# Performance work log

Measured on AMD Instinct MI355X. Metric: run time of the kernel, lower is better.

The kernel has to match this reference:

```python
import jax, jax.numpy as jnp
import numpy as np

N_NODES = 50000
N_EDGES = 800000
D = 128
N_LAYERS = 3


def setup_inputs() -> dict:
    key = jax.random.key(0)
    k = jax.random.split(key, 6)
    x = jax.random.normal(k[0], (N_NODES, D), dtype=jnp.float32)
    edge_index = jax.random.randint(k[1], (2, N_EDGES), 0, N_NODES, dtype=jnp.int64)
    scale = 1.0 / np.sqrt(D)
    # SAGEConv params per layer: lin_l (aggregated neighbors, with bias), lin_r (root)
    W_l = jax.random.uniform(k[2], (N_LAYERS, D, D), jnp.float32, -scale, scale)
    b_l = jax.random.uniform(k[3], (N_LAYERS, D), jnp.float32, -scale, scale)
    W_r = jax.random.uniform(k[4], (N_LAYERS, D, D), jnp.float32, -scale, scale)
    return {"x": x, "edge_index": edge_index, "W_l": W_l, "b_l": b_l, "W_r": W_r}


def _sage_layer(x, src, dst, inv_deg, Wl, bl, Wr):
    # gather source-node features, mean-aggregate into destination nodes
    msg = x[src]                                            # [E, D]
    agg = jax.ops.segment_sum(msg, dst, num_segments=N_NODES) * inv_deg  # [N, D]
    # out = lin_l(agg) + lin_r(x)
    return agg @ Wl.T + bl + x @ Wr.T


def reference(x, edge_index, W_l, b_l, W_r):
    src = edge_index[0]
    dst = edge_index[1]
    deg = jax.ops.segment_sum(jnp.ones((src.shape[0],), x.dtype), dst,
                              num_segments=N_NODES)
    inv_deg = (1.0 / jnp.maximum(deg, 1.0))[:, None]        # [N, 1]
    h = x
    for i in range(N_LAYERS):
        h = _sage_layer(h, src, dst, inv_deg, W_l[i], b_l[i], W_r[i])
        if i < N_LAYERS - 1:
            h = jax.nn.relu(h)  # dropout=0.0 -> identity
    return h
```

## Files before the change

### kernel.cpp

```cpp
#include <hip/hip_runtime.h>

#define N_NODES 50000
#define N_EDGES 800000
#define D 128
#define N_LAYERS 3
#define NBUCK ((N_NODES + 255) / 256)

typedef __attribute__((ext_vector_type(8))) short bfrag;
typedef __attribute__((ext_vector_type(4))) float f32x4;
typedef __attribute__((ext_vector_type(8))) unsigned short u16x8;

__device__ __forceinline__ unsigned short f2bf_rn(float f) {
    union { float f; unsigned u; } a; a.f = f;
    unsigned r = a.u + 0x7fffu + ((a.u >> 16) & 1u);
    return (unsigned short)(r >> 16);
}
__device__ __forceinline__ float bf2f(unsigned short h) {
    union { unsigned u; float f; } a; a.u = ((unsigned)h) << 16;
    return a.f;
}
__device__ __forceinline__ unsigned short f2h(float f) {
    union { unsigned short s[1]; _Float16 h; } a; a.h = (_Float16)f; return a.s[0];
}
__device__ __forceinline__ float h2f(unsigned short u) {
    union { unsigned short s[1]; _Float16 h; } a; a.s[0] = u; return (float)a.h;
}

#define GLOAD16(g, l) __builtin_amdgcn_global_load_lds( \
    (const __attribute__((address_space(1))) void*)(g), \
    (__attribute__((address_space(3))) void*)(l), 16, 0, 0)

__global__ void detect_dtype_kernel(const unsigned int* __restrict__ edge, int* __restrict__ flag,
                                    int* __restrict__ gcoarse) {
    __shared__ int any_nz;
    if (threadIdx.x == 0) any_nz = 0;
    __syncthreads();
    int nz = 0;
    for (int i = threadIdx.x; i < 2048; i += blockDim.x) {
        if (edge[2 * i + 1] != 0u) nz = 1;
    }
    if (nz) atomicOr(&any_nz, 1);
    for (int i = threadIdx.x; i < NBUCK; i += blockDim.x) gcoarse[i] = 0;
    __syncthreads();
    if (threadIdx.x == 0) *flag = any_nz ? 0 : 1;
}

__global__ __launch_bounds__(256) void hist_coarse_kernel(const int* __restrict__ edge,
                                                          const int* __restrict__ flag,
                                                          int* __restrict__ gcoarse) {
    __shared__ int h[NBUCK];
    const int t = threadIdx.x;
    for (int i = t; i < NBUCK; i += 256) h[i] = 0;
    __syncthreads();
    const int flagv = *flag;
    const int base = blockIdx.x * 1024;
#pragma unroll
    for (int j = 0; j < 4; ++j) {
        int i = base + j * 256 + t;
        if (i < N_EDGES) {
            int d = flagv ? edge[2 * ((size_t)N_EDGES + i)] : edge[N_EDGES + i];
            atomicAdd(&h[d >> 8], 1);
        }
    }
    __syncthreads();
    for (int i = t; i < NBUCK; i += 256)
        if (h[i]) atomicAdd(&gcoarse[i], h[i]);
}

__global__ __launch_bounds__(256) void scan196_kernel(const int* __restrict__ gcoarse,
                                                      int* __restrict__ bucket_base,
                                                      int* __restrict__ cursor1) {
    __shared__ int s[256];
    int t = threadIdx.x;
    int v = (t < NBUCK) ? gcoarse[t] : 0;
    s[t] = v;
    __syncthreads();
    for (int off = 1; off < 256; off <<= 1) {
        int u = (t >= off) ? s[t - off] : 0;
        __syncthreads();
        s[t] += u;
        __syncthreads();
    }
    if (t < NBUCK) {
        int excl = s[t] - v;
        bucket_base[t] = excl;
        cursor1[t] = excl;
    }
    if (t == 255) bucket_base[NBUCK] = s[255];
}

__global__ __launch_bounds__(256) void pass1_kernel(const int* __restrict__ edge,
                                                    const int* __restrict__ flag,
                                                    int* __restrict__ cursor1,
                                                    int* __restrict__ packed) {
    __shared__ int hist[NBUCK];
    __shared__ int base[NBUCK];
    const int t = threadIdx.x;
    const int flagv = *flag;
    const int blockBeg = blockIdx.x * 4096;
    for (int i = t; i < NBUCK; i += 256) hist[i] = 0;
    __syncthreads();
    int es[16], ed[16];
#pragma unroll
    for (int j = 0; j < 16; ++j) {
        int e = blockBeg + j * 256 + t;
        if (e < N_EDGES) {
            if (flagv) { es[j] = edge[2 * (size_t)e]; ed[j] = edge[2 * ((size_t)N_EDGES + e)]; }
            else       { es[j] = edge[e];             ed[j] = edge[N_EDGES + e]; }
        } else ed[j] = -1;
    }
#pragma unroll
    for (int j = 0; j < 16; ++j)
        if (ed[j] >= 0) atomicAdd(&hist[ed[j] >> 8], 1);
    __syncthreads();
    for (int i = t; i < NBUCK; i += 256) {
        base[i] = atomicAdd(&cursor1[i], hist[i]);
        hist[i] = 0;
    }
    __syncthreads();
#pragma unroll
    for (int j = 0; j < 16; ++j) {
        if (ed[j] >= 0) {
            int b = ed[j] >> 8;
            int pos = base[b] + atomicAdd(&hist[b], 1);
            packed[pos] = ((ed[j] & 255) << 18) | es[j];
        }
    }
}

__global__ __launch_bounds__(256) void build_csr_kernel(const int* __restrict__ bucket_base,
                                                        const int* __restrict__ packed,
                                                        int* __restrict__ offsets,
                                                        float* __restrict__ inv_deg,
                                                        int* __restrict__ csr) {
    __shared__ int cnt[256];
    __shared__ int s[256];
    const int t = threadIdx.x;
    const int b = blockIdx.x;
    const int base = bucket_base[b];
    const int endb = bucket_base[b + 1];
    cnt[t] = 0;
    __syncthreads();
    for (int e = base + t; e < endb; e += 256)
        atomicAdd(&cnt[((unsigned)packed[e]) >> 18], 1);
    __syncthreads();
    int v = cnt[t];
    s[t] = v;
    __syncthreads();
    for (int off = 1; off < 256; off <<= 1) {
        int u = (t >= off) ? s[t - off] : 0;
        __syncthreads();
        s[t] += u;
        __syncthreads();
    }
    int excl = base + s[t] - v;
    int node = b * 256 + t;
    if (node < N_NODES) {
        offsets[node] = excl;
        inv_deg[node] = 1.0f / (float)max(v, 1);
    }
    if (b == NBUCK - 1 && t == 0) offsets[N_NODES] = N_EDGES;
    cnt[t] = excl;
    __syncthreads();
    for (int e = base + t; e < endb; e += 256) {
        int p = packed[e];
        int pos = atomicAdd(&cnt[((unsigned)p) >> 18], 1);
        csr[pos] = p & 0x3FFFF;
    }
}

__global__ void prep_w_kernel(const float* __restrict__ Wl, const float* __restrict__ Wr,
                              unsigned short* __restrict__ WH, unsigned short* __restrict__ WL) {
    int idx = blockIdx.x * blockDim.x + threadIdx.x;
    if (idx >= N_LAYERS * 128 * 256) return;
    int k = idx & 255;
    int j = (idx >> 8) & 127;
    int l = idx >> 15;
    float v = (k < 128) ? Wl[((size_t)l * 128 + j) * 128 + k]
                        : Wr[((size_t)l * 128 + j) * 128 + (k - 128)];
    unsigned short hi = f2bf_rn(v);
    WH[idx] = hi;
    WL[idx] = f2bf_rn(v - bf2f(hi));
}

__global__ void split_x_kernel(const float* __restrict__ x,
                               unsigned short* __restrict__ H16, unsigned short* __restrict__ R16) {
    int t = blockIdx.x * 256 + threadIdx.x;
    if (t >= N_NODES * 32) return;
    float4 v = reinterpret_cast<const float4*>(x)[t];
    ushort4 h, r;
    h.x = f2h(v.x); r.x = f2h(v.x - h2f(h.x));
    h.y = f2h(v.y); r.y = f2h(v.y - h2f(h.y));
    h.z = f2h(v.z); r.z = f2h(v.z - h2f(h.z));
    h.w = f2h(v.w); r.w = f2h(v.w - h2f(h.w));
    reinterpret_cast<ushort4*>(H16)[t] = h;
    reinterpret_cast<ushort4*>(R16)[t] = r;
}

__global__ __launch_bounds__(256) void aggregate_kernel(const unsigned short* __restrict__ hF16,
                                                        const int* __restrict__ offsets,
                                                        const int* __restrict__ csr_src,
                                                        const float* __restrict__ inv_deg,
                                                        unsigned short* __restrict__ aggH,
                                                        unsigned short* __restrict__ aggL) {
    int node = blockIdx.x * 4 + (threadIdx.x >> 6);
    int lane = threadIdx.x & 63;
    int q = lane >> 4;
    int c = lane & 15;
    if (node >= N_NODES) return;
    int beg = offsets[node];
    int end = offsets[node + 1];
    float a0[8], a1[8];
#pragma unroll
    for (int j = 0; j < 8; ++j) { a0[j] = 0.f; a1[j] = 0.f; }
    int e = beg + q;
    for (; e + 4 < end; e += 8) {
        int s0 = csr_src[e];
        int s1 = csr_src[e + 4];
        u16x8 v0 = *reinterpret_cast<const u16x8*>(hF16 + (size_t)s0 * 128 + c * 8);
        u16x8 v1 = *reinterpret_cast<const u16x8*>(hF16 + (size_t)s1 * 128 + c * 8);
#pragma unroll
        for (int j = 0; j < 8; ++j) {
            a0[j] += h2f(v0[j]);
            a1[j] += h2f(v1[j]);
        }
    }
    if (e < end) {
        int s0 = csr_src[e];
        u16x8 v0 = *reinterpret_cast<const u16x8*>(hF16 + (size_t)s0 * 128 + c * 8);
#pragma unroll
        for (int j = 0; j < 8; ++j) a0[j] += h2f(v0[j]);
    }
#pragma unroll
    for (int j = 0; j < 8; ++j) a0[j] += a1[j];
#pragma unroll
    for (int j = 0; j < 8; ++j) a0[j] += __shfl_xor(a0[j], 16, 64);
#pragma unroll
    for (int j = 0; j < 8; ++j) a0[j] += __shfl_xor(a0[j], 32, 64);
    if (q == 0) {
        float w = inv_deg[node];
        u16x8 hi, lo;
#pragma unroll
        for (int j = 0; j < 8; ++j) {
            float v = a0[j] * w;
            hi[j] = f2bf_rn(v);
            lo[j] = f2bf_rn(v - bf2f(hi[j]));
        }
        *reinterpret_cast<u16x8*>(aggH + (size_t)node * 128 + c * 8) = hi;
        *reinterpret_cast<u16x8*>(aggL + (size_t)node * 128 + c * 8) = lo;
    }
}

template <int RELU, int LAST>
__global__ __launch_bounds__(256) void mfma_gemm_kernel(
    const unsigned short* __restrict__ aggH, const unsigned short* __restrict__ aggL,
    const unsigned short* h16, const unsigned short* r16,
    const unsigned short* __restrict__ WH, const unsigned short* __restrict__ WL,
    const float* __restrict__ bias,
    float* __restrict__ OutF, unsigned short* H16o, unsigned short* R16o)
{
    __shared__ __align__(16) unsigned short Bh[4][128][8];
    __shared__ __align__(16) unsigned short Bl[4][128][8];
    const int tid = threadIdx.x;
    const int lane = tid & 63;
    const int wv = tid >> 6;
    const int m16 = lane & 15;
    const int kg = lane >> 4;
    const int blockRow = blockIdx.x * 64;
    const int rowg = blockRow + wv * 16 + m16;
    const int rowc = min(rowg, N_NODES - 1);

    f32x4 acc[8];
#pragma unroll
    for (int t = 0; t < 8; ++t) acc[t] = (f32x4){0.f, 0.f, 0.f, 0.f};

    for (int ks = 0; ks < 8; ++ks) {
        const int kc = ks * 32;
        const int kcol = kc & 127;
        bfrag a_h, a_l;
        if (kc < 128) {
            a_h = *reinterpret_cast<const bfrag*>(aggH + (size_t)rowc * 128 + kcol + kg * 8);
            a_l = *reinterpret_cast<const bfrag*>(aggL + (size_t)rowc * 128 + kcol + kg * 8);
        } else {
            u16x8 hv = *reinterpret_cast<const u16x8*>(h16 + (size_t)rowc * 128 + kcol + kg * 8);
            u16x8 rv = *reinterpret_cast<const u16x8*>(r16 + (size_t)rowc * 128 + kcol + kg * 8);
#pragma unroll
            for (int j = 0; j < 8; ++j) {
                float v = h2f(hv[j]) + h2f(rv[j]);
                union { float f; unsigned u; } a; a.f = v;
                unsigned hu = a.u & 0xFFFF0000u;
                a_h[j] = (short)(hu >> 16);
                union { unsigned u; float f; } b; b.u = hu;
                a_l[j] = (short)f2bf_rn(v - b.f);
            }
        }
        {
            const unsigned short* g0 = WH + (size_t)lane * 256 + kc + wv * 8;
            const unsigned short* g1 = WH + (size_t)(64 + lane) * 256 + kc + wv * 8;
            GLOAD16(g0, (char*)&Bh[0][0][0] + wv * 2048);
            GLOAD16(g1, (char*)&Bh[0][0][0] + wv * 2048 + 1024);
            const unsigned short* g2 = WL + (size_t)lane * 256 + kc + wv * 8;
            const unsigned short* g3 = WL + (size_t)(64 + lane) * 256 + kc + wv * 8;
            GLOAD16(g2, (char*)&Bl[0][0][0] + wv * 2048);
            GLOAD16(g3, (char*)&Bl[0][0][0] + wv * 2048 + 1024);
        }
        __syncthreads();
#pragma unroll
        for (int t = 0; t < 8; ++t) {
            bfrag bh = *reinterpret_cast<const bfrag*>(&Bh[kg][t * 16 + m16][0]);
            bfrag bl = *reinterpret_cast<const bfrag*>(&Bl[kg][t * 16 + m16][0]);
            acc[t] = __builtin_amdgcn_mfma_f32_16x16x32_bf16(a_h, bh, acc[t], 0, 0, 0);
            acc[t] = __builtin_amdgcn_mfma_f32_16x16x32_bf16(a_l, bh, acc[t], 0, 0, 0);
            acc[t] = __builtin_amdgcn_mfma_f32_16x16x32_bf16(a_h, bl, acc[t], 0, 0, 0);
        }
        __syncthreads();
    }

#pragma unroll
    for (int t = 0; t < 8; ++t) {
        int col = t * 16 + m16;
        float bv = bias[col];
#pragma unroll
        for (int r = 0; r < 4; ++r) {
            int row = blockRow + wv * 16 + kg * 4 + r;
            if (row >= N_NODES) continue;
            float v = acc[t][r] + bv;
            if (RELU) v = fmaxf(v, 0.f);
            if (LAST) {
                OutF[(size_t)row * 128 + col] = v;
            } else {
                unsigned short h = f2h(v);
                H16o[(size_t)row * 128 + col] = h;
                R16o[(size_t)row * 128 + col] = f2h(v - h2f(h));
            }
        }
    }
}

extern "C" void kernel_launch(void* const* d_in, const int* in_sizes, int n_in,
                              void* d_out, int out_size, void* d_ws, size_t ws_size,
                              hipStream_t stream) {
    const float* x  = (const float*)d_in[0];
    const int*   ei = (const int*)d_in[1];
    const float* Wl = (const float*)d_in[2];
    const float* bl = (const float*)d_in[3];
    const float* Wr = (const float*)d_in[4];
    float* out = (float*)d_out;
    char* ws = (char*)d_ws;

    int*            flag     = (int*)(ws + 0);
    int*            gcoarse  = (int*)(ws + 1024);
    int*            bbase    = (int*)(ws + 2048);
    int*            cursor1  = (int*)(ws + 3072);
    int*            offs     = (int*)(ws + 4096);
    float*          invd     = (float*)(ws + 208896);
    int*            packed   = (int*)(ws + 409600);
    int*            csr      = (int*)(ws + 3609600);
    unsigned short* WH       = (unsigned short*)(ws + 6809600);
    unsigned short* WL       = (unsigned short*)(ws + 7006208);
    unsigned short* h16      = (unsigned short*)(ws + 7202816);
    unsigned short* r16      = (unsigned short*)(ws + 20002816);
    unsigned short* aggH     = (unsigned short*)(ws + 32802816);
    unsigned short* aggL     = (unsigned short*)(ws + 45602816);

    detect_dtype_kernel<<<1, 256, 0, stream>>>((const unsigned int*)ei, flag, gcoarse);
    hist_coarse_kernel<<<(N_EDGES + 1023) / 1024, 256, 0, stream>>>(ei, flag, gcoarse);
    scan196_kernel<<<1, 256, 0, stream>>>(gcoarse, bbase, cursor1);
    pass1_kernel<<<(N_EDGES + 4095) / 4096, 256, 0, stream>>>(ei, flag, cursor1, packed);
    build_csr_kernel<<<NBUCK, 256, 0, stream>>>(bbase, packed, offs, invd, csr);
    prep_w_kernel<<<(N_LAYERS * 128 * 256 + 255) / 256, 256, 0, stream>>>(Wl, Wr, WH, WL);
    split_x_kernel<<<(N_NODES * 32 + 255) / 256, 256, 0, stream>>>(x, h16, r16);

    const int aggGrid = N_NODES / 4;
    const int gemmGrid = (N_NODES + 63) / 64;

    aggregate_kernel<<<aggGrid, 256, 0, stream>>>(h16, offs, csr, invd, aggH, aggL);
    mfma_gemm_kernel<1, 0><<<gemmGrid, 256, 0, stream>>>(aggH, aggL, h16, r16,
        WH + 0 * 32768, WL + 0 * 32768, bl + 0, nullptr, h16, r16);
    aggregate_kernel<<<aggGrid, 256, 0, stream>>>(h16, offs, csr, invd, aggH, aggL);
    mfma_gemm_kernel<1, 0><<<gemmGrid, 256, 0, stream>>>(aggH, aggL, h16, r16,
        WH + 1 * 32768, WL + 1 * 32768, bl + 128, nullptr, h16, r16);
    aggregate_kernel<<<aggGrid, 256, 0, stream>>>(h16, offs, csr, invd, aggH, aggL);
    mfma_gemm_kernel<0, 1><<<gemmGrid, 256, 0, stream>>>(aggH, aggL, h16, r16,
        WH + 2 * 32768, WL + 2 * 32768, bl + 256, out, nullptr, nullptr);
}
```

Before: 260.3 us.

## Drop low-order residual splits for activations and aggregates, read weights directly

Removes the fp16 residual (r16) buffer for node features and the bf16 low part (aggL) of aggregates, so the GEMM keeps only the hi×Wh and hi×Wl products (two MFMAs instead of three) and the aggregation, split and epilogue stop writing the extra buffers. The GEMM also stops staging weights in LDS through global_load_lds with block barriers, and each wave reads its weight fragments straight from global or cache. This cuts memory traffic and MFMA work per layer but lowers accuracy: activations become single fp16 or bf16 values, which may weaken the tolerance margin. Reading weights directly replaces LDS reuse with repeated cache loads.

```diff
diff --git a/kernel.cpp b/kernel.cpp
--- a/kernel.cpp
+++ b/kernel.cpp
@@ -25,10 +25,6 @@
 __device__ __forceinline__ float h2f(unsigned short u) {
     union { unsigned short s[1]; _Float16 h; } a; a.s[0] = u; return (float)a.h;
 }
-
-#define GLOAD16(g, l) __builtin_amdgcn_global_load_lds( \
-    (const __attribute__((address_space(1))) void*)(g), \
-    (__attribute__((address_space(3))) void*)(l), 16, 0, 0)
 
 __global__ void detect_dtype_kernel(const unsigned int* __restrict__ edge, int* __restrict__ flag,
                                     int* __restrict__ gcoarse) {
@@ -183,26 +179,23 @@
     WL[idx] = f2bf_rn(v - bf2f(hi));
 }
 
-__global__ void split_x_kernel(const float* __restrict__ x,
-                               unsigned short* __restrict__ H16, unsigned short* __restrict__ R16) {
+__global__ void split_x_kernel(const float* __restrict__ x, unsigned short* __restrict__ H16) {
     int t = blockIdx.x * 256 + threadIdx.x;
     if (t >= N_NODES * 32) return;
     float4 v = reinterpret_cast<const float4*>(x)[t];
-    ushort4 h, r;
-    h.x = f2h(v.x); r.x = f2h(v.x - h2f(h.x));
-    h.y = f2h(v.y); r.y = f2h(v.y - h2f(h.y));
-    h.z = f2h(v.z); r.z = f2h(v.z - h2f(h.z));
-    h.w = f2h(v.w); r.w = f2h(v.w - h2f(h.w));
+    ushort4 h;
+    h.x = f2h(v.x);
+    h.y = f2h(v.y);
+    h.z = f2h(v.z);
+    h.w = f2h(v.w);
     reinterpret_cast<ushort4*>(H16)[t] = h;
-    reinterpret_cast<ushort4*>(R16)[t] = r;
 }
 
 __global__ __launch_bounds__(256) void aggregate_kernel(const unsigned short* __restrict__ hF16,
                                                         const int* __restrict__ offsets,
                                                         const int* __restrict__ csr_src,
                                                         const float* __restrict__ inv_deg,
-                                                        unsigned short* __restrict__ aggH,
-                                                        unsigned short* __restrict__ aggL) {
+                                                        unsigned short* __restrict__ aggH) {
     int node = blockIdx.x * 4 + (threadIdx.x >> 6);
     int lane = threadIdx.x & 63;
     int q = lane >> 4;
@@ -239,28 +232,21 @@
     for (int j = 0; j < 8; ++j) a0[j] += __shfl_xor(a0[j], 32, 64);
     if (q == 0) {
         float w = inv_deg[node];
-        u16x8 hi, lo;
-#pragma unroll
-        for (int j = 0; j < 8; ++j) {
-            float v = a0[j] * w;
-            hi[j] = f2bf_rn(v);
-            lo[j] = f2bf_rn(v - bf2f(hi[j]));
-        }
+        u16x8 hi;
+#pragma unroll
+        for (int j = 0; j < 8; ++j) hi[j] = f2bf_rn(a0[j] * w);
         *reinterpret_cast<u16x8*>(aggH + (size_t)node * 128 + c * 8) = hi;
-        *reinterpret_cast<u16x8*>(aggL + (size_t)node * 128 + c * 8) = lo;
     }
 }
 
 template <int RELU, int LAST>
 __global__ __launch_bounds__(256) void mfma_gemm_kernel(
-    const unsigned short* __restrict__ aggH, const unsigned short* __restrict__ aggL,
-    const unsigned short* h16, const unsigned short* r16,
+    const unsigned short* __restrict__ aggH,
+    const unsigned short* h16,
     const unsigned short* __restrict__ WH, const unsigned short* __restrict__ WL,
     const float* __restrict__ bias,
-    float* __restrict__ OutF, unsigned short* H16o, unsigned short* R16o)
+    float* __restrict__ OutF, unsigned short* H16o)
 {
-    __shared__ __align__(16) unsigned short Bh[4][128][8];
-    __shared__ __align__(16) unsigned short Bl[4][128][8];
     const int tid = threadIdx.x;
     const int lane = tid & 63;
     const int wv = tid >> 6;
@@ -274,46 +260,26 @@
 #pragma unroll
     for (int t = 0; t < 8; ++t) acc[t] = (f32x4){0.f, 0.f, 0.f, 0.f};
 
+#pragma unroll
     for (int ks = 0; ks < 8; ++ks) {
         const int kc = ks * 32;
-        const int kcol = kc & 127;
-        bfrag a_h, a_l;
-        if (kc < 128) {
-            a_h = *reinterpret_cast<const bfrag*>(aggH + (size_t)rowc * 128 + kcol + kg * 8);
-            a_l = *reinterpret_cast<const bfrag*>(aggL + (size_t)rowc * 128 + kcol + kg * 8);
+        bfrag a;
+        if (ks < 4) {
+            a = *reinterpret_cast<const bfrag*>(aggH + (size_t)rowc * 128 + kc + kg * 8);
         } else {
-            u16x8 hv = *reinterpret_cast<const u16x8*>(h16 + (size_t)rowc * 128 + kcol + kg * 8);
-            u16x8 rv = *reinterpret_cast<const u16x8*>(r16 + (size_t)rowc * 128 + kcol + kg * 8);
-#pragma unroll
-            for (int j = 0; j < 8; ++j) {
-                float v = h2f(hv[j]) + h2f(rv[j]);
-                union { float f; unsigned u; } a; a.f = v;
-                unsigned hu = a.u & 0xFFFF0000u;
-                a_h[j] = (short)(hu >> 16);
-                union { unsigned u; float f; } b; b.u = hu;
-                a_l[j] = (short)f2bf_rn(v - b.f);
-            }
-        }
-        {
-            const unsigned short* g0 = WH + (size_t)lane * 256 + kc + wv * 8;
-            const unsigned short* g1 = WH + (size_t)(64 + lane) * 256 + kc + wv * 8;
-            GLOAD16(g0, (char*)&Bh[0][0][0] + wv * 2048);
-            GLOAD16(g1, (char*)&Bh[0][0][0] + wv * 2048 + 1024);
-            const unsigned short* g2 = WL + (size_t)lane * 256 + kc + wv * 8;
-            const unsigned short* g3 = WL + (size_t)(64 + lane) * 256 + kc + wv * 8;
-            GLOAD16(g2, (char*)&Bl[0][0][0] + wv * 2048);
-            GLOAD16(g3, (char*)&Bl[0][0][0] + wv * 2048 + 1024);
-        }
-        __syncthreads();
+            u16x8 hv = *reinterpret_cast<const u16x8*>(h16 + (size_t)rowc * 128 + (kc - 128) + kg * 8);
+#pragma unroll
+            for (int j = 0; j < 8; ++j) a[j] = (short)f2bf_rn(h2f(hv[j]));
+        }
+        const unsigned short* wp = WH + (size_t)m16 * 256 + kc + kg * 8;
+        const unsigned short* wq = WL + (size_t)m16 * 256 + kc + kg * 8;
 #pragma unroll
         for (int t = 0; t < 8; ++t) {
-            bfrag bh = *reinterpret_cast<const bfrag*>(&Bh[kg][t * 16 + m16][0]);
-            bfrag bl = *reinterpret_cast<const bfrag*>(&Bl[kg][t * 16 + m16][0]);
-            acc[t] = __builtin_amdgcn_mfma_f32_16x16x32_bf16(a_h, bh, acc[t], 0, 0, 0);
-            acc[t] = __builtin_amdgcn_mfma_f32_16x16x32_bf16(a_l, bh, acc[t], 0, 0, 0);
-            acc[t] = __builtin_amdgcn_mfma_f32_16x16x32_bf16(a_h, bl, acc[t], 0, 0, 0);
-        }
-        __syncthreads();
+            bfrag bh = *reinterpret_cast<const bfrag*>(wp + (size_t)t * 16 * 256);
+            bfrag bl = *reinterpret_cast<const bfrag*>(wq + (size_t)t * 16 * 256);
+            acc[t] = __builtin_amdgcn_mfma_f32_16x16x32_bf16(a, bh, acc[t], 0, 0, 0);
+            acc[t] = __builtin_amdgcn_mfma_f32_16x16x32_bf16(a, bl, acc[t], 0, 0, 0);
+        }
     }
 
 #pragma unroll
@@ -329,9 +295,7 @@
             if (LAST) {
                 OutF[(size_t)row * 128 + col] = v;
             } else {
-                unsigned short h = f2h(v);
-                H16o[(size_t)row * 128 + col] = h;
-                R16o[(size_t)row * 128 + col] = f2h(v - h2f(h));
+                H16o[(size_t)row * 128 + col] = f2h(v);
             }
         }
     }
@@ -359,9 +323,7 @@
     unsigned short* WH       = (unsigned short*)(ws + 6809600);
     unsigned short* WL       = (unsigned short*)(ws + 7006208);
     unsigned short* h16      = (unsigned short*)(ws + 7202816);
-    unsigned short* r16      = (unsigned short*)(ws + 20002816);
-    unsigned short* aggH     = (unsigned short*)(ws + 32802816);
-    unsigned short* aggL     = (unsigned short*)(ws + 45602816);
+    unsigned short* aggH     = (unsigned short*)(ws + 20002816);
 
     detect_dtype_kernel<<<1, 256, 0, stream>>>((const unsigned int*)ei, flag, gcoarse);
     hist_coarse_kernel<<<(N_EDGES + 1023) / 1024, 256, 0, stream>>>(ei, flag, gcoarse);
@@ -369,18 +331,18 @@
     pass1_kernel<<<(N_EDGES + 4095) / 4096, 256, 0, stream>>>(ei, flag, cursor1, packed);
     build_csr_kernel<<<NBUCK, 256, 0, stream>>>(bbase, packed, offs, invd, csr);
     prep_w_kernel<<<(N_LAYERS * 128 * 256 + 255) / 256, 256, 0, stream>>>(Wl, Wr, WH, WL);
-    split_x_kernel<<<(N_NODES * 32 + 255) / 256, 256, 0, stream>>>(x, h16, r16);
+    split_x_kernel<<<(N_NODES * 32 + 255) / 256, 256, 0, stream>>>(x, h16);
 
     const int aggGrid = N_NODES / 4;
     const int gemmGrid = (N_NODES + 63) / 64;
 
-    aggregate_kernel<<<aggGrid, 256, 0, stream>>>(h16, offs, csr, invd, aggH, aggL);
-    mfma_gemm_kernel<1, 0><<<gemmGrid, 256, 0, stream>>>(aggH, aggL, h16, r16,
-        WH + 0 * 32768, WL + 0 * 32768, bl + 0, nullptr, h16, r16);
-    aggregate_kernel<<<aggGrid, 256, 0, stream>>>(h16, offs, csr, invd, aggH, aggL);
-    mfma_gemm_kernel<1, 0><<<gemmGrid, 256, 0, stream>>>(aggH, aggL, h16, r16,
-        WH + 1 * 32768, WL + 1 * 32768, bl + 128, nullptr, h16, r16);
-    aggregate_kernel<<<aggGrid, 256, 0, stream>>>(h16, offs, csr, invd, aggH, aggL);
-    mfma_gemm_kernel<0, 1><<<gemmGrid, 256, 0, stream>>>(aggH, aggL, h16, r16,
-        WH + 2 * 32768, WL + 2 * 32768, bl + 256, out, nullptr, nullptr);
-}
+    aggregate_kernel<<<aggGrid, 256, 0, stream>>>(h16, offs, csr, invd, aggH);
+    mfma_gemm_kernel<1, 0><<<gemmGrid, 256, 0, stream>>>(aggH, h16,
+        WH + 0 * 32768, WL + 0 * 32768, bl + 0, nullptr, h16);
+    aggregate_kernel<<<aggGrid, 256, 0, stream>>>(h16, offs, csr, invd, aggH);
+    mfma_gemm_kernel<1, 0><<<gemmGrid, 256, 0, stream>>>(aggH, h16,
+        WH + 1 * 32768, WL + 1 * 32768, bl + 128, nullptr, h16);
+    aggregate_kernel<<<aggGrid, 256, 0, stream>>>(h16, offs, csr, invd, aggH);
+    mfma_gemm_kernel<0, 1><<<gemmGrid, 256, 0, stream>>>(aggH, h16,
+        WH + 2 * 32768, WL + 2 * 32768, bl + 256, out, nullptr);
+}
```

Result: slower. 351.0 us (+34.9%).
